# Kernel tuning notes

Hardware: AMD Instinct MI355X
Metric: run time of the kernel (lower is better)

Reference implementation:

```python
import jax, jax.numpy as jnp
import numpy as np
from jax import lax

S, B, W = 128, 64, 16          # sent_len, batch, word_len
V, CV = 50000, 100             # word vocab, char vocab
WE, CE, FN, CK = 300, 30, 4, 3 # word emb dim, char emb dim, char filter num, char kernel
C = 512                        # cnn_out_channel
NT = 20                        # number of tags
NL = 3                         # number of GLU conv layers
PAD = 0


def setup_inputs() -> dict:
    key = jax.random.key(0)
    ks = jax.random.split(key, 16)
    words = jax.random.randint(ks[0], (S, B), 1, V)          # no pads -> full CRF mask
    chars = jax.random.randint(ks[1], (B, S, W), 1, CV)
    tags = jax.random.randint(ks[2], (S, B), 0, NT)
    word_emb = jax.random.normal(ks[3], (V, WE), jnp.float32) * 0.1
    char_emb = jax.random.normal(ks[4], (CV, CE), jnp.float32) * 0.1
    char_cnn_w = jax.random.normal(ks[5], (CE * FN, 1, CK), jnp.float32) * 0.1  # grouped conv, groups=CE
    char_cnn_b = jax.random.normal(ks[6], (CE * FN,), jnp.float32) * 0.01
    lin_w = jax.random.normal(ks[7], (WE + CE * FN, C), jnp.float32) * 0.05
    lin_b = jax.random.normal(ks[8], (C,), jnp.float32) * 0.01
    conv_w = jax.random.normal(ks[9], (NL, 2 * C, C, 3), jnp.float32) * 0.03
    conv_b = jax.random.normal(ks[10], (NL, 2 * C), jnp.float32) * 0.01
    fc_w = jax.random.normal(ks[11], (C, NT), jnp.float32) * 0.05
    fc_b = jax.random.normal(ks[12], (NT,), jnp.float32) * 0.01
    crf_start = jax.random.normal(ks[13], (NT,), jnp.float32) * 0.1
    crf_end = jax.random.normal(ks[14], (NT,), jnp.float32) * 0.1
    crf_trans = jax.random.normal(ks[15], (NT, NT), jnp.float32) * 0.1
    return dict(words=words, chars=chars, tags=tags, word_emb=word_emb, char_emb=char_emb,
                char_cnn_w=char_cnn_w, char_cnn_b=char_cnn_b, lin_w=lin_w, lin_b=lin_b,
                conv_w=conv_w, conv_b=conv_b, fc_w=fc_w, fc_b=fc_b,
                crf_start=crf_start, crf_end=crf_end, crf_trans=crf_trans)


def _emissions(words, chars, word_emb, char_emb, char_cnn_w, char_cnn_b,
               lin_w, lin_b, conv_w, conv_b, fc_w, fc_b):
    s, b = words.shape
    # word embeddings: [S,B,WE]
    emb_out = word_emb[words]
    # char embeddings + batched grouped char-CNN (replaces the python loop over sent positions)
    ch = char_emb[chars]                                   # [B,S,W,CE]
    ch = ch.reshape(b * s, W, CE).transpose(0, 2, 1)       # [B*S, CE, W]
    co = lax.conv_general_dilated(ch, char_cnn_w, (1,), 'VALID',
                                  dimension_numbers=('NCH', 'OIH', 'NCH'),
                                  feature_group_count=CE)
    co = co + char_cnn_b[None, :, None]                    # [B*S, CE*FN, W-CK+1]
    cf = co.max(axis=2).reshape(b, s, CE * FN).transpose(1, 0, 2)  # [S,B,120]
    word_features = jnp.concatenate([emb_out, cf], axis=2)  # [S,B,420]
    # gated-CNN (GLU) encoder
    h = word_features @ lin_w + lin_b                      # [S,B,C]
    h = jnp.transpose(h, (1, 2, 0))                        # [B,C,S]
    scale = jnp.sqrt(jnp.asarray(0.5, h.dtype))
    for l in range(conv_w.shape[0]):
        c = lax.conv_general_dilated(h, conv_w[l], (1,), ((1, 1),),
                                     dimension_numbers=('NCH', 'OIH', 'NCH'))
        c = c + conv_b[l][None, :, None]                   # [B,2C,S]
        a, g = jnp.split(c, 2, axis=1)
        h = (a * jax.nn.sigmoid(g) + h) * scale            # GLU + residual + scale
    enc = jnp.transpose(h, (2, 0, 1))                      # [S,B,C]
    emis = enc @ fc_w + fc_b                               # [S,B,NT]
    mask = (words != PAD)                                  # [S,B]
    return emis, mask


def _crf_nll(emis, tags, mask, crf_start, crf_end, crf_trans):
    s, b, nt = emis.shape
    maskf = mask.astype(emis.dtype)
    bi = jnp.arange(b)
    # numerator: score of the gold path
    emis_sc = jnp.take_along_axis(emis, tags[:, :, None], axis=2)[..., 0]  # [S,B]
    trans_sc = crf_trans[tags[:-1], tags[1:]]                              # [S-1,B]
    num = crf_start[tags[0]] + emis_sc[0] + ((trans_sc + emis_sc[1:]) * maskf[1:]).sum(0)
    last_idx = mask.sum(0).astype(jnp.int32) - 1
    num = num + crf_end[tags[last_idx, bi]]
    # denominator: forward algorithm (sequential DP over time)
    alpha0 = crf_start[None, :] + emis[0]                  # [B,NT]
    def step(alpha, xs):
        e_t, m_t = xs
        nxt = jax.nn.logsumexp(alpha[:, :, None] + crf_trans[None] + e_t[:, None, :], axis=1)
        return jnp.where(m_t[:, None], nxt, alpha), None
    alpha, _ = lax.scan(step, alpha0, (emis[1:], mask[1:]))
    logz = jax.nn.logsumexp(alpha + crf_end[None, :], axis=1)
    return -(num - logz).sum()


def _viterbi(emis, mask, crf_start, crf_end, crf_trans):
    s, b, nt = emis.shape
    bi = jnp.arange(b)
    ident = jnp.broadcast_to(jnp.arange(nt)[None, :], (b, nt))
    score0 = crf_start[None, :] + emis[0]                  # [B,NT]
    def step(score, xs):
        e_t, m_t = xs
        brd = score[:, :, None] + crf_trans[None]          # [B,NT_prev,NT_cur]
        bp = jnp.argmax(brd, axis=1)                       # [B,NT]
        nxt = jnp.max(brd, axis=1) + e_t
        score = jnp.where(m_t[:, None], nxt, score)
        bp = jnp.where(m_t[:, None], bp, ident)
        return score, bp
    final, bps = lax.scan(step, score0, (emis[1:], mask[1:]))  # bps [S-1,B,NT]
    last_tag = jnp.argmax(final + crf_end[None, :], axis=1)    # [B]
    def back(tag, bp):
        prev = bp[bi, tag]
        return prev, tag
    first_tag, rest = lax.scan(back, last_tag, bps, reverse=True)  # rest: tags at 1..S-1
    return jnp.concatenate([first_tag[None], rest], axis=0).astype(jnp.int32)  # [S,B]


def reference(words, chars, tags, word_emb, char_emb, char_cnn_w, char_cnn_b,
              lin_w, lin_b, conv_w, conv_b, fc_w, fc_b, crf_start, crf_end, crf_trans):
    emis, mask = _emissions(words, chars, word_emb, char_emb, char_cnn_w, char_cnn_b,
                            lin_w, lin_b, conv_w, conv_b, fc_w, fc_b)
    crf_out = _viterbi(emis, mask, crf_start, crf_end, crf_trans)
    crf_loss = _crf_nll(emis, tags, mask, crf_start, crf_end, crf_trans)
    return crf_out, crf_loss
```

## Files before the change

### kernel.cpp

```cpp
#include <hip/hip_runtime.h>
#include <math.h>

typedef unsigned short ushort_t;
typedef short bf16x8 __attribute__((ext_vector_type(8)));
typedef float f32x4 __attribute__((ext_vector_type(4)));
typedef unsigned short u16x8 __attribute__((ext_vector_type(8)));

#define S_ 128
#define B_ 64
#define W_ 16
#define CE_ 30
#define FN_ 4
#define WE_ 300
#define FEAT_ 420
#define C_ 512
#define NT_ 20
#define KL_ 448

#define LOG2E_ 1.44269504088896340736f
#define LN2_   0.69314718055994530942f

#define EM_OFF   0
#define NLL_OFF  163840
#define H0_OFF   163968
#define HBUF_F   2129920
#define H1_OFF   (H0_OFF + HBUF_F)
#define WS_OFF   (H1_OFF + HBUF_F)
#define WSP_F    2359296
#define LW_OFF   (WS_OFF + WSP_F)
#define FS_OFF   (LW_OFF + 114688)
#define FW_OFF   (FS_OFF + 1835008)
#define WLAYER   (1024*1536)

__device__ __forceinline__ float b2f(ushort_t h) {
    unsigned u = ((unsigned)h) << 16;
    float f; __builtin_memcpy(&f, &u, 4); return f;
}
__device__ __forceinline__ ushort_t f2b(float f) {
    unsigned u; __builtin_memcpy(&u, &f, 4);
    unsigned r = (u + 0x7FFFu + ((u >> 16) & 1u)) >> 16;
    return (ushort_t)r;
}
__device__ __forceinline__ void gload16(const void* g, void* l) {
    __builtin_amdgcn_global_load_lds((const __attribute__((address_space(1))) void*)g,
                                     (__attribute__((address_space(3))) void*)l,
                                     16, 0, 0);
}

__global__ void k_embed(const int* __restrict__ words,
                        const float* __restrict__ word_emb,
                        const int* __restrict__ chars,
                        const float* __restrict__ char_emb,
                        const float* __restrict__ cw,
                        const float* __restrict__ cb,
                        ushort_t* __restrict__ Fh) {
    const int n = blockIdx.x;
    const int t = threadIdx.x;
    {
        int s = n >> 6, b = n & 63;
        int np = b * 128 + s;
        int wid = words[n];
        if (t < WE_ / 4) {
            float4 v = ((const float4*)(word_emb + (size_t)wid * WE_))[t];
            ushort4 o;
            o.x = f2b(v.x); o.y = f2b(v.y); o.z = f2b(v.z); o.w = f2b(v.w);
            *(ushort4*)(Fh + (size_t)np * KL_ + t * 4) = o;
        }
    }
    {
        int b = n >> 7, s = n & 127;
        int np = b * 128 + s;
        __shared__ int cidx[W_];
        if (t < W_) cidx[t] = chars[n * W_ + t];
        __syncthreads();
        if (t < CE_ * FN_) {
            int g = t >> 2;
            float w0 = cw[t*3+0], w1 = cw[t*3+1], w2 = cw[t*3+2];
            float x[W_];
            #pragma unroll
            for (int j = 0; j < W_; ++j) x[j] = char_emb[cidx[j] * CE_ + g];
            float m = -INFINITY;
            #pragma unroll
            for (int j = 0; j < W_ - 2; ++j) {
                float v = x[j]*w0 + x[j+1]*w1 + x[j+2]*w2;
                m = fmaxf(m, v);
            }
            Fh[(size_t)np * KL_ + WE_ + t] = f2b(m + cb[t]);
        }
        if (t < KL_ - FEAT_) Fh[(size_t)np * KL_ + FEAT_ + t] = 0;
    }
}

__global__ void k_prep(const float* __restrict__ conv_w, ushort_t* __restrict__ Wt,
                       const float* __restrict__ lin_w,  ushort_t* __restrict__ Lh,
                       const float* __restrict__ fc_w,   float* __restrict__ fwT,
                       ushort_t* __restrict__ h0, ushort_t* __restrict__ h1) {
    const int bid = blockIdx.x;
    const int t = threadIdx.x;
    if (bid < 18432) {
        size_t i = (size_t)bid * 256 + t;
        int ci = (int)(i & 511);
        int kr = (int)((i >> 9) % 3);
        size_t lo_ = i / 1536;
        Wt[i] = f2b(conv_w[lo_ * 1536 + (size_t)ci * 3 + kr]);
    } else if (bid < 19328) {
        int idx = (bid - 18432) * 256 + t;
        int c = idx / KL_, k = idx - c * KL_;
        float v = (k < FEAT_) ? lin_w[(size_t)k * C_ + c] : 0.f;
        Lh[idx] = f2b(v);
    } else if (bid < 19368) {
        int idx = (bid - 19328) * 256 + t;
        if (idx < NT_ * C_) {
            int j = idx >> 9, c = idx & 511;
            fwT[idx] = fc_w[(size_t)c * NT_ + j];
        }
    } else {
        int r = bid - 19368;
        int b = r >> 2, which = r & 3;
        ushort_t* buf = (which & 1) ? h1 : h0;
        int row = (which >> 1) ? 129 : 0;
        ((unsigned*)(buf + ((size_t)b * 130 + row) * 512))[t] = 0u;
    }
}

__global__ __launch_bounds__(256) void k_lin_gemm(
    const ushort_t* __restrict__ Lh, const ushort_t* __restrict__ Fh,
    const float* __restrict__ lb, ushort_t* __restrict__ Oh)
{
    __shared__ short lds[8192];
    short* AhS = lds;
    short* BhS = lds + 4096;

    const int bid = blockIdx.x;
    const int c0 = (bid & 3) << 7;
    const int n0 = (bid >> 2) << 7;
    const int t = threadIdx.x;
    const int w = t >> 6;
    const int lane = t & 63;
    const int wr = w >> 1, wc = w & 1;

    const int srow0 = (w << 5) + (lane >> 2);
    const int srow1 = srow0 + 16;
    const int j0 = (lane & 3) ^ ((srow0 >> 1) & 3);
    const int j1 = (lane & 3) ^ ((srow1 >> 1) & 3);
    const size_t aoff0 = (size_t)(c0 + srow0) * KL_ + j0 * 8;
    const size_t aoff1 = (size_t)(c0 + srow1) * KL_ + j1 * 8;
    const size_t boff0 = (size_t)(n0 + srow0) * KL_ + j0 * 8;
    const size_t boff1 = (size_t)(n0 + srow1) * KL_ + j1 * 8;
    const int wofs = w << 10;

    const int lr = lane & 15, kg = lane >> 4;
    int aro[4], bro[4];
    #pragma unroll
    for (int m = 0; m < 4; ++m) { int r = (wr << 6) + (m << 4) + lr; aro[m] = (r << 5) + ((kg ^ ((r >> 1) & 3)) << 3); }
    #pragma unroll
    for (int n = 0; n < 4; ++n) { int r = (wc << 6) + (n << 4) + lr; bro[n] = (r << 5) + ((kg ^ ((r >> 1) & 3)) << 3); }

    f32x4 acc[4][4];
    #pragma unroll
    for (int m = 0; m < 4; ++m)
        #pragma unroll
        for (int n = 0; n < 4; ++n) acc[m][n] = (f32x4){0.f, 0.f, 0.f, 0.f};

    for (int k0 = 0; k0 < KL_; k0 += 32) {
        gload16(Lh + aoff0 + k0, AhS + wofs);
        gload16(Lh + aoff1 + k0, AhS + wofs + 512);
        gload16(Fh + boff0 + k0, BhS + wofs);
        gload16(Fh + boff1 + k0, BhS + wofs + 512);
        __syncthreads();
        bf16x8 avh[4], bvh[4];
        #pragma unroll
        for (int m = 0; m < 4; ++m) avh[m] = *(const bf16x8*)(AhS + aro[m]);
        #pragma unroll
        for (int n = 0; n < 4; ++n) bvh[n] = *(const bf16x8*)(BhS + bro[n]);
        #pragma unroll
        for (int m = 0; m < 4; ++m)
            #pragma unroll
            for (int n = 0; n < 4; ++n)
                acc[m][n] = __builtin_amdgcn_mfma_f32_16x16x32_bf16(avh[m], bvh[n], acc[m][n], 0, 0, 0);
        __syncthreads();
    }

    #pragma unroll
    for (int m = 0; m < 4; ++m) {
        const int c = c0 + (wr << 6) + (m << 4) + (kg << 2);
        float4 bb = *(const float4*)(lb + c);
        #pragma unroll
        for (int n = 0; n < 4; ++n) {
            const int np = n0 + (wc << 6) + (n << 4) + lr;
            const int b = np >> 7, s = np & 127;
            ushort4 h4;
            h4.x = f2b(acc[m][n][0] + bb.x);
            h4.y = f2b(acc[m][n][1] + bb.y);
            h4.z = f2b(acc[m][n][2] + bb.z);
            h4.w = f2b(acc[m][n][3] + bb.w);
            *(ushort4*)(Oh + ((size_t)b * 130 + s + 1) * 512 + c) = h4;
        }
    }
}

#define CBUFS 16896
__global__ __launch_bounds__(256) void k_conv_gemm(
    const ushort_t* __restrict__ Wt, const ushort_t* __restrict__ Ht,
    const float* __restrict__ cb,
    ushort_t* __restrict__ Ot)
{
    __shared__ short lds2[2 * CBUFS];
    float* g_lds = (float*)lds2;

    const int bid  = blockIdx.x;
    const int co0  = (bid >> 6) << 6;
    const int b    = bid & 63;
    const int t    = threadIdx.x;
    const int w    = t >> 6;
    const int lane = t & 63;
    const int wr   = w >> 1;
    const int wc   = w & 1;

    const int srow0 = (w << 5) + (lane >> 2);
    const int srow1 = srow0 + 16;
    const int j0 = (lane & 3) ^ ((srow0 >> 1) & 3);
    const int j1 = (lane & 3) ^ ((srow1 >> 1) & 3);
    const int coA0 = (srow0 < 64) ? (co0 + srow0) : (512 + co0 + srow0 - 64);
    const int coA1 = (srow1 < 64) ? (co0 + srow1) : (512 + co0 + srow1 - 64);
    const size_t aoff0 = (size_t)coA0 * 1536 + j0 * 8;
    const size_t aoff1 = (size_t)coA1 * 1536 + j1 * 8;
    const int lrow = lane >> 2;
    const int wofs = w << 10;

    const int lr = lane & 15, kg = lane >> 4;
    int aro[4];
    #pragma unroll
    for (int m = 0; m < 4; ++m) { int r = (wr << 6) + (m << 4) + lr; aro[m] = (r << 5) + ((kg ^ ((r >> 1) & 3)) << 3); }
    int bro[3][4];
    #pragma unroll
    for (int kr = 0; kr < 3; ++kr)
        #pragma unroll
        for (int n = 0; n < 4; ++n) {
            int r = (wc << 6) + (n << 4) + lr + kr;
            bro[kr][n] = (r << 5) + ((kg ^ ((r >> 1) & 3)) << 3);
        }

    f32x4 acc[4][4];
    #pragma unroll
    for (int m = 0; m < 4; ++m)
        #pragma unroll
        for (int n = 0; n < 4; ++n) acc[m][n] = (f32x4){0.f, 0.f, 0.f, 0.f};

    {
        short* AS = lds2;
        short* BS = lds2 + 12288;
        #pragma unroll
        for (int kr = 0; kr < 3; ++kr) {
            gload16(Wt + aoff0 + kr * 512, AS + kr * 4096 + wofs);
            gload16(Wt + aoff1 + kr * 512, AS + kr * 4096 + wofs + 512);
        }
        for (int i = w; i < 9; i += 4) {
            const int rr = (i << 4) + lrow;
            const int sj = (lane & 3) ^ ((rr >> 1) & 3);
            gload16(Ht + ((size_t)b * 130 + rr) * 512 + sj * 8, BS + (i << 9));
        }
    }
    __syncthreads();

    for (int it = 0; it < 16; ++it) {
        const int cur = it & 1;
        if (it + 1 < 16) {
            const int ci0 = (it + 1) << 5;
            short* ASn = lds2 + (cur ^ 1) * CBUFS;
            short* BSn = ASn + 12288;
            #pragma unroll
            for (int kr = 0; kr < 3; ++kr) {
                gload16(Wt + aoff0 + kr * 512 + ci0, ASn + kr * 4096 + wofs);
                gload16(Wt + aoff1 + kr * 512 + ci0, ASn + kr * 4096 + wofs + 512);
            }
            for (int i = w; i < 9; i += 4) {
                const int rr = (i << 4) + lrow;
                const int sj = (lane & 3) ^ ((rr >> 1) & 3);
                gload16(Ht + ((size_t)b * 130 + rr) * 512 + ci0 + sj * 8, BSn + (i << 9));
            }
        }
        const short* AS = lds2 + cur * CBUFS;
        const short* BS = AS + 12288;
        #pragma unroll
        for (int kr = 0; kr < 3; ++kr) {
            const short* A_h = AS + kr * 4096;
            bf16x8 avh[4], bvh[4];
            #pragma unroll
            for (int m = 0; m < 4; ++m) avh[m] = *(const bf16x8*)(A_h + aro[m]);
            #pragma unroll
            for (int n = 0; n < 4; ++n) bvh[n] = *(const bf16x8*)(BS + bro[kr][n]);
            #pragma unroll
            for (int m = 0; m < 4; ++m)
                #pragma unroll
                for (int n = 0; n < 4; ++n)
                    acc[m][n] = __builtin_amdgcn_mfma_f32_16x16x32_bf16(avh[m], bvh[n], acc[m][n], 0, 0, 0);
        }
        __syncthreads();
    }

    const float rs = 0.70710678118654752f;
    if (wr == 1) {
        #pragma unroll
        for (int m = 0; m < 4; ++m) {
            const int co_l = (m << 4) + (kg << 2);
            float4 bg = *(const float4*)(cb + 512 + co0 + co_l);
            #pragma unroll
            for (int n = 0; n < 4; ++n) {
                const int s_l = (wc << 6) + (n << 4) + lr;
                float4 gv;
                gv.x = acc[m][n][0] + bg.x;
                gv.y = acc[m][n][1] + bg.y;
                gv.z = acc[m][n][2] + bg.z;
                gv.w = acc[m][n][3] + bg.w;
                *(float4*)&g_lds[s_l * 68 + co_l] = gv;
            }
        }
    }
    __syncthreads();
    if (wr == 0) {
        #pragma unroll
        for (int m = 0; m < 4; ++m) {
            const int co_l = (m << 4) + (kg << 2);
            float4 ba = *(const float4*)(cb + co0 + co_l);
            #pragma unroll
            for (int n = 0; n < 4; ++n) {
                const int s_l = (wc << 6) + (n << 4) + lr;
                float4 gv = *(const float4*)&g_lds[s_l * 68 + co_l];
                size_t dst = ((size_t)b * 130 + s_l + 1) * 512 + co0 + co_l;
                ushort4 rh = *(const ushort4*)(Ht + dst);
                float a0 = acc[m][n][0] + ba.x, g0 = gv.x;
                float a1 = acc[m][n][1] + ba.y, g1 = gv.y;
                float a2 = acc[m][n][2] + ba.z, g2 = gv.z;
                float a3 = acc[m][n][3] + ba.w, g3 = gv.w;
                ushort4 h4;
                h4.x = f2b((a0 / (1.f + expf(-g0)) + b2f(rh.x)) * rs);
                h4.y = f2b((a1 / (1.f + expf(-g1)) + b2f(rh.y)) * rs);
                h4.z = f2b((a2 / (1.f + expf(-g2)) + b2f(rh.z)) * rs);
                h4.w = f2b((a3 / (1.f + expf(-g3)) + b2f(rh.w)) * rs);
                *(ushort4*)(Ot + dst) = h4;
            }
        }
    }
}

__global__ __launch_bounds__(256) void k_emis3(const ushort_t* __restrict__ hh,
                                               const float* __restrict__ fwT,
                                               const float* __restrict__ fc_b,
                                               float* __restrict__ emis) {
    __shared__ short hlds[16 * 520];
    __shared__ float wlds[20 * 516];
    const int b  = blockIdx.y;
    const int sc = blockIdx.x;
    const int t  = threadIdx.x;
    const int w  = t >> 6, lane = t & 63;

    #pragma unroll
    for (int i = 0; i < 4; ++i) {
        int r = w * 4 + i;
        gload16(hh + ((size_t)b * 130 + sc * 16 + r + 1) * 512 + lane * 8,
                hlds + r * 520);
    }
    for (int idx = t; idx < 20 * 128; idx += 256) {
        int j = idx >> 7, cq = (idx & 127) << 2;
        *(float4*)&wlds[j * 516 + cq] = *(const float4*)(fwT + j * 512 + cq);
    }
    __syncthreads();

    #pragma unroll
    for (int pass = 0; pass < 2; ++pass) {
        int slot = t + pass * 256;
        if (slot < 16 * NT_) {
            int r = slot / NT_, j = slot - r * NT_;
            const short* hp = hlds + r * 520;
            const float* wp = wlds + j * 516;
            float acc = 0.f;
            for (int c0 = 0; c0 < 512; c0 += 8) {
                u16x8 hv = *(const u16x8*)(hp + c0);
                float4 w0 = *(const float4*)(wp + c0);
                float4 w1 = *(const float4*)(wp + c0 + 4);
                acc += b2f(hv[0])*w0.x + b2f(hv[1])*w0.y + b2f(hv[2])*w0.z + b2f(hv[3])*w0.w
                     + b2f(hv[4])*w1.x + b2f(hv[5])*w1.y + b2f(hv[6])*w1.z + b2f(hv[7])*w1.w;
            }
            int s = sc * 16 + r;
            emis[((size_t)s * B_ + b) * NT_ + j] = acc + fc_b[j];
        }
    }
}

#define VMAX(a, b) __builtin_elementwise_max((a), (b))
#define MAX20T(mx, a0, a1, a2, a3, a4) \
    { f32x4 mv_ = VMAX(VMAX(VMAX(a0, a1), VMAX(a2, a3)), a4); \
      mx = fmaxf(fmaxf(mv_[0], mv_[1]), fmaxf(mv_[2], mv_[3])); }
#define SEL(ov, oi, av, ai, bv2, bi2) \
    { bool g_ = (bv2) > (av); ov = g_ ? (bv2) : (av); oi = g_ ? (bi2) : (ai); }
#define ARGMAX20(best, bi, v0, v1, v2, v3, v4) \
    { float p0v,p1v,p2v,p3v,p4v,p5v,p6v,p7v,p8v,p9v; \
      int   p0i,p1i,p2i,p3i,p4i,p5i,p6i,p7i,p8i,p9i; \
      SEL(p0v,p0i, v0[0],0,  v0[1],1);  SEL(p1v,p1i, v0[2],2,  v0[3],3); \
      SEL(p2v,p2i, v1[0],4,  v1[1],5);  SEL(p3v,p3i, v1[2],6,  v1[3],7); \
      SEL(p4v,p4i, v2[0],8,  v2[1],9);  SEL(p5v,p5i, v2[2],10, v2[3],11); \
      SEL(p6v,p6i, v3[0],12, v3[1],13); SEL(p7v,p7i, v3[2],14, v3[3],15); \
      SEL(p8v,p8i, v4[0],16, v4[1],17); SEL(p9v,p9i, v4[2],18, v4[3],19); \
      float q0v,q1v,q2v,q3v,q4v; int q0i,q1i,q2i,q3i,q4i; \
      SEL(q0v,q0i,p0v,p0i,p1v,p1i); SEL(q1v,q1i,p2v,p2i,p3v,p3i); \
      SEL(q2v,q2i,p4v,p4i,p5v,p5i); SEL(q3v,q3i,p6v,p6i,p7v,p7i); \
      SEL(q4v,q4i,p8v,p8i,p9v,p9i); \
      float r0v,r1v; int r0i,r1i; \
      SEL(r0v,r0i,q0v,q0i,q1v,q1i); SEL(r1v,r1i,q2v,q2i,q3v,q3i); \
      float s0v; int s0i; \
      SEL(s0v,s0i,r0v,r0i,r1v,r1i); \
      SEL(best,bi,s0v,s0i,q4v,q4i); }
#define EXPC(d, s) d[0]=__builtin_amdgcn_exp2f(s[0]*LOG2E_); d[1]=__builtin_amdgcn_exp2f(s[1]*LOG2E_); \
                   d[2]=__builtin_amdgcn_exp2f(s[2]*LOG2E_); d[3]=__builtin_amdgcn_exp2f(s[3]*LOG2E_)
#define LGKM0() asm volatile("s_waitcnt lgkmcnt(0)" ::: "memory")

__global__ __launch_bounds__(256) void k_crf(const float* __restrict__ emis,
                                             const int* __restrict__ words,
                                             const int* __restrict__ tags,
                                             const float* __restrict__ tstart,
                                             const float* __restrict__ tend,
                                             const float* __restrict__ ttrans,
                                             float* __restrict__ nll,
                                             float* __restrict__ out) {
    __shared__ float e_lds[S_ * NT_];
    __shared__ float pe_lds[S_ * NT_];
    __shared__ int   P_lds[S_ * NT_];
    __shared__ float brA[32], brB[32], brC[32], brD[32];
    __shared__ float Fv[NT_], Gv[NT_], a63[NT_], g63[NT_];
    __shared__ float CfL, CbL;
    __shared__ int tag63L;
    const int b = blockIdx.x;
    const int t = threadIdx.x;
    const int w = t >> 6;
    const int ln = t & 63;

    for (int idx = t; idx < S_ * NT_; idx += 256) {
        int tt = idx / NT_, j = idx - tt * NT_;
        float ev = emis[((size_t)tt * B_ + b) * NT_ + j];
        e_lds[idx] = ev;
        pe_lds[idx] = __builtin_amdgcn_exp2f(ev * LOG2E_);
    }
    __syncthreads();

    unsigned long long mlo = __ballot(words[ln * B_ + b] != 0);
    unsigned long long mhi = __ballot(words[(64 + ln) * B_ + b] != 0);
    const bool act = ln < NT_;
    const int jc = act ? ln : 0;
    float part = 0.f;

    #define MBIT(tt) ((((tt) < 64 ? (mlo >> (tt)) : (mhi >> ((tt) - 64))) & 1ull) != 0)

    if (w == 0) {
        for (int tt = ln; tt < S_; tt += 64) {
            int tgc = tags[tt * B_ + b];
            bool m = MBIT(tt);
            if (tt == 0) {
                part += tstart[tgc] + e_lds[tgc];
            } else if (m) {
                int tgp = tags[(tt - 1) * B_ + b];
                part += ttrans[tgp * NT_ + tgc] + e_lds[tt * NT_ + tgc];
            }
        }
        #pragma unroll
        for (int o = 32; o >= 1; o >>= 1) part += __shfl_down(part, o);

        f32x4 t0, t1, t2, t3, t4;
        #define LDTC(v, q) v = (f32x4){ ttrans[(4*(q)+0)*NT_ + jc], ttrans[(4*(q)+1)*NT_ + jc], \
                                        ttrans[(4*(q)+2)*NT_ + jc], ttrans[(4*(q)+3)*NT_ + jc] }
        LDTC(t0, 0); LDTC(t1, 1); LDTC(t2, 2); LDTC(t3, 3); LDTC(t4, 4);
        f32x4 E0, E1, E2, E3, E4;
        EXPC(E0, t0); EXPC(E1, t1); EXPC(E2, t2); EXPC(E3, t3); EXPC(E4, t4);

        float a0own = tstart[jc] + e_lds[jc];
        if (act) brA[ln] = a0own;
        LGKM0();
        f32x4 a0 = *(const f32x4*)&brA[0];
        f32x4 a1 = *(const f32x4*)&brA[4];
        f32x4 a2 = *(const f32x4*)&brA[8];
        f32x4 a3 = *(const f32x4*)&brA[12];
        f32x4 a4 = *(const f32x4*)&brA[16];
        float m0; MAX20T(m0, a0, a1, a2, a3, a4);
        float beta = __builtin_amdgcn_exp2f((a0own - m0) * LOG2E_);
        int L2 = 0;
        for (int tt = 1; tt < 64; ++tt) {
            if (MBIT(tt)) {
                float pe = pe_lds[tt * NT_ + jc];
                if (act) brA[ln] = beta;
                LGKM0();
                f32x4 b0 = *(const f32x4*)&brA[0];
                f32x4 b1 = *(const f32x4*)&brA[4];
                f32x4 b2 = *(const f32x4*)&brA[8];
                f32x4 b3 = *(const f32x4*)&brA[12];
                f32x4 b4 = *(const f32x4*)&brA[16];
                float mx; MAX20T(mx, b0, b1, b2, b3, b4);
                f32x4 pr = b0 * E0 + b1 * E1 + b2 * E2 + b3 * E3 + b4 * E4;
                float dot = (pr[0] + pr[1]) + (pr[2] + pr[3]);
                unsigned bits; __builtin_memcpy(&bits, &mx, 4);
                int ex = (int)((bits >> 23) & 255u) - 127;
                unsigned rb = (unsigned)(127 - ex) << 23;
                float r; __builtin_memcpy(&r, &rb, 4);
                L2 += ex;
                beta = dot * r * pe;
            }
        }
        if (act) Fv[ln] = beta;
        if (ln == 0) CfL = m0 + (float)L2 * LN2_;
    } else if (w == 1) {
        f32x4 r0, r1, r2, r3, r4;
        #define LDTR(v, q) v = (f32x4){ ttrans[jc*NT_ + 4*(q)+0], ttrans[jc*NT_ + 4*(q)+1], \
                                        ttrans[jc*NT_ + 4*(q)+2], ttrans[jc*NT_ + 4*(q)+3] }
        LDTR(r0, 0); LDTR(r1, 1); LDTR(r2, 2); LDTR(r3, 3); LDTR(r4, 4);
        f32x4 E0, E1, E2, E3, E4;
        EXPC(E0, r0); EXPC(E1, r1); EXPC(E2, r2); EXPC(E3, r3); EXPC(E4, r4);
        f32x4 d0 = (f32x4){ tend[0],  tend[1],  tend[2],  tend[3]  };
        f32x4 d1 = (f32x4){ tend[4],  tend[5],  tend[6],  tend[7]  };
        f32x4 d2 = (f32x4){ tend[8],  tend[9],  tend[10], tend[11] };
        f32x4 d3 = (f32x4){ tend[12], tend[13], tend[14], tend[15] };
        f32x4 d4 = (f32x4){ tend[16], tend[17], tend[18], tend[19] };
        float mend; MAX20T(mend, d0, d1, d2, d3, d4);
        float G = __builtin_amdgcn_exp2f((tend[jc] - mend) * LOG2E_);
        int L2b = 0;
        for (int tt = 126; tt >= 63; --tt) {
            if (MBIT(tt + 1)) {
                float w_own = G * pe_lds[(tt + 1) * NT_ + jc];
                if (act) brB[ln] = w_own;
                LGKM0();
                f32x4 q0 = *(const f32x4*)&brB[0];
                f32x4 q1 = *(const f32x4*)&brB[4];
                f32x4 q2 = *(const f32x4*)&brB[8];
                f32x4 q3 = *(const f32x4*)&brB[12];
                f32x4 q4 = *(const f32x4*)&brB[16];
                float mx; MAX20T(mx, q0, q1, q2, q3, q4);
                f32x4 pr = q0 * E0 + q1 * E1 + q2 * E2 + q3 * E3 + q4 * E4;
                float dot = (pr[0] + pr[1]) + (pr[2] + pr[3]);
                unsigned bits; __builtin_memcpy(&bits, &mx, 4);
                int ex = (int)((bits >> 23) & 255u) - 127;
                unsigned rb = (unsigned)(127 - ex) << 23;
                float r; __builtin_memcpy(&r, &rb, 4);
                L2b += ex;
                G = dot * r;
            }
        }
        if (act) Gv[ln] = G;
        if (ln == 0) CbL = mend + (float)L2b * LN2_;
    } else if (w == 2) {
        f32x4 t0, t1, t2, t3, t4;
        LDTC(t0, 0); LDTC(t1, 1); LDTC(t2, 2); LDTC(t3, 3); LDTC(t4, 4);
        float sown = tstart[jc] + e_lds[jc];
        if (act) brC[ln] = sown;
        LGKM0();
        for (int tt = 1; tt < 64; ++tt) {
            float e = e_lds[tt * NT_ + jc];
            f32x4 a0 = *(const f32x4*)&brC[0];
            f32x4 a1 = *(const f32x4*)&brC[4];
            f32x4 a2 = *(const f32x4*)&brC[8];
            f32x4 a3 = *(const f32x4*)&brC[12];
            f32x4 a4 = *(const f32x4*)&brC[16];
            f32x4 v0 = a0 + t0, v1 = a1 + t1, v2 = a2 + t2, v3 = a3 + t3, v4 = a4 + t4;
            float best; int bi;
            ARGMAX20(best, bi, v0, v1, v2, v3, v4);
            bool m = MBIT(tt);
            float nxt = best + e;
            sown = m ? nxt : sown;
            if (act) {
                brC[ln] = sown;
                P_lds[tt * NT_ + ln] = m ? bi : ln;
            }
            LGKM0();
        }
        if (act) a63[ln] = sown;
    } else {
        f32x4 r0, r1, r2, r3, r4;
        LDTR(r0, 0); LDTR(r1, 1); LDTR(r2, 2); LDTR(r3, 3); LDTR(r4, 4);
        float gown = tend[jc];
        if (act) brD[ln] = gown + e_lds[127 * NT_ + jc];
        LGKM0();
        for (int tt = 126; tt >= 63; --tt) {
            f32x4 q0 = *(const f32x4*)&brD[0];
            f32x4 q1 = *(const f32x4*)&brD[4];
            f32x4 q2 = *(const f32x4*)&brD[8];
            f32x4 q3 = *(const f32x4*)&brD[12];
            f32x4 q4 = *(const f32x4*)&brD[16];
            f32x4 v0 = r0 + q0, v1 = r1 + q1, v2 = r2 + q2, v3 = r3 + q3, v4 = r4 + q4;
            float best; int bi;
            ARGMAX20(best, bi, v0, v1, v2, v3, v4);
            bool m = MBIT(tt + 1);
            gown = m ? best : gown;
            if (act) {
                P_lds[(tt + 1) * NT_ + ln] = m ? bi : ln;
                brD[ln] = gown + e_lds[tt * NT_ + jc];
            }
            LGKM0();
        }
        if (act) g63[ln] = gown;
    }
    __syncthreads();

    if (t == 0) {
        float zf = 0.f;
        #pragma unroll
        for (int j = 0; j < NT_; ++j) zf += Fv[j] * Gv[j];
        float logz = CfL + CbL + __builtin_amdgcn_logf(zf) * LN2_;
        int cnt = __popcll(mlo) + __popcll(mhi);
        float num = part + tend[tags[(cnt - 1) * B_ + b]];
        nll[b] = logz - num;
        float bv = a63[0] + g63[0]; int bt = 0;
        #pragma unroll
        for (int j = 1; j < NT_; ++j) {
            float v = a63[j] + g63[j];
            if (v > bv) { bv = v; bt = j; }
        }
        tag63L = bt;
    }
    __syncthreads();

    if (t == 128) {
        int tag = tag63L;
        out[63 * B_ + b] = (float)tag;
        for (int tt = 63; tt >= 1; --tt) {
            tag = P_lds[tt * NT_ + tag];
            out[(tt - 1) * B_ + b] = (float)tag;
        }
    }
    if (t == 192) {
        int tag = tag63L;
        for (int tt = 64; tt < 128; ++tt) {
            tag = P_lds[tt * NT_ + tag];
            out[tt * B_ + b] = (float)tag;
        }
    }
}

__global__ void k_loss(const float* __restrict__ nll, float* __restrict__ out) {
    float v = nll[threadIdx.x];
    #pragma unroll
    for (int o = 32; o >= 1; o >>= 1) v += __shfl_down(v, o);
    if (threadIdx.x == 0) out[S_ * B_] = v;
}

extern "C" void kernel_launch(void* const* d_in, const int* in_sizes, int n_in,
                              void* d_out, int out_size, void* d_ws, size_t ws_size,
                              hipStream_t stream) {
    (void)in_sizes; (void)n_in; (void)out_size; (void)ws_size;
    const int*   words     = (const int*)d_in[0];
    const int*   chars     = (const int*)d_in[1];
    const int*   tags      = (const int*)d_in[2];
    const float* word_emb  = (const float*)d_in[3];
    const float* char_emb  = (const float*)d_in[4];
    const float* ccw       = (const float*)d_in[5];
    const float* ccb       = (const float*)d_in[6];
    const float* lin_w     = (const float*)d_in[7];
    const float* lin_b     = (const float*)d_in[8];
    const float* conv_w    = (const float*)d_in[9];
    const float* conv_b    = (const float*)d_in[10];
    const float* fc_w      = (const float*)d_in[11];
    const float* fc_b      = (const float*)d_in[12];
    const float* crf_start = (const float*)d_in[13];
    const float* crf_end   = (const float*)d_in[14];
    const float* crf_trans = (const float*)d_in[15];

    float* ws   = (float*)d_ws;
    float* em   = ws + EM_OFF;
    float* nll  = ws + NLL_OFF;
    ushort_t* h0  = (ushort_t*)(ws + H0_OFF);
    ushort_t* h1  = (ushort_t*)(ws + H1_OFF);
    ushort_t* wsp = (ushort_t*)(ws + WS_OFF);
    ushort_t* lwp = (ushort_t*)(ws + LW_OFF);
    ushort_t* fsp = (ushort_t*)(ws + FS_OFF);
    float* fwT  = ws + FW_OFF;
    float* out  = (float*)d_out;

    k_embed<<<S_ * B_, 128, 0, stream>>>(words, word_emb, chars, char_emb, ccw, ccb, fsp);
    k_prep<<<19624, 256, 0, stream>>>(conv_w, wsp, lin_w, lwp, fc_w, fwT, h0, h1);
    k_lin_gemm<<<256, 256, 0, stream>>>(lwp, fsp, lin_b, h0);

    k_conv_gemm<<<512, 256, 0, stream>>>(wsp,              h0, conv_b,        h1);
    k_conv_gemm<<<512, 256, 0, stream>>>(wsp + WLAYER,     h1, conv_b + 1024, h0);
    k_conv_gemm<<<512, 256, 0, stream>>>(wsp + 2*WLAYER,   h0, conv_b + 2048, h1);

    k_emis3<<<dim3(8, B_), 256, 0, stream>>>(h1, fwT, fc_b, em);
    k_crf<<<B_, 256, 0, stream>>>(em, words, tags, crf_start, crf_end, crf_trans, nll, out);
    k_loss<<<1, 64, 0, stream>>>(nll, out);
}
```

Baseline: 173.9 us.

## Load conv GEMM weight fragments directly into registers instead of LDS

The GLU conv GEMM kernel stops staging the weight (A) tiles through shared memory. Each lane now reads its MFMA A fragments straight from global memory into a double-buffered register array, and only the activation (B) tiles stay double-buffered in LDS, which shrinks the shared-memory footprint. The aim is to cut LDS traffic and footprint, which could allow higher occupancy. The cost is more VGPRs (96 extra bf16x8 registers), a fully unrolled loop, and non-coalesced 16-byte global reads per lane that may expose load latency.

Result: slower. 252.7 us (+45.4%).

```diff
diff --git a/kernel.cpp b/kernel.cpp
--- a/kernel.cpp
+++ b/kernel.cpp
@@ -199,14 +199,13 @@
     }
 }
 
-#define CBUFS 16896
 __global__ __launch_bounds__(256) void k_conv_gemm(
     const ushort_t* __restrict__ Wt, const ushort_t* __restrict__ Ht,
     const float* __restrict__ cb,
     ushort_t* __restrict__ Ot)
 {
-    __shared__ short lds2[2 * CBUFS];
-    float* g_lds = (float*)lds2;
+    __shared__ short ldsB[17408];
+    float* g_lds = (float*)ldsB;
 
     const int bid  = blockIdx.x;
     const int co0  = (bid >> 6) << 6;
@@ -217,21 +216,16 @@
     const int wr   = w >> 1;
     const int wc   = w & 1;
 
-    const int srow0 = (w << 5) + (lane >> 2);
-    const int srow1 = srow0 + 16;
-    const int j0 = (lane & 3) ^ ((srow0 >> 1) & 3);
-    const int j1 = (lane & 3) ^ ((srow1 >> 1) & 3);
-    const int coA0 = (srow0 < 64) ? (co0 + srow0) : (512 + co0 + srow0 - 64);
-    const int coA1 = (srow1 < 64) ? (co0 + srow1) : (512 + co0 + srow1 - 64);
-    const size_t aoff0 = (size_t)coA0 * 1536 + j0 * 8;
-    const size_t aoff1 = (size_t)coA1 * 1536 + j1 * 8;
     const int lrow = lane >> 2;
-    const int wofs = w << 10;
-
     const int lr = lane & 15, kg = lane >> 4;
-    int aro[4];
-    #pragma unroll
-    for (int m = 0; m < 4; ++m) { int r = (wr << 6) + (m << 4) + lr; aro[m] = (r << 5) + ((kg ^ ((r >> 1) & 3)) << 3); }
+
+    const ushort_t* aP[4];
+    #pragma unroll
+    for (int m = 0; m < 4; ++m) {
+        int r = (wr << 6) + (m << 4) + lr;
+        int coA = (r < 64) ? (co0 + r) : (512 + co0 + r - 64);
+        aP[m] = Wt + (size_t)coA * 1536 + kg * 8;
+    }
     int bro[3][4];
     #pragma unroll
     for (int kr = 0; kr < 3; ++kr)
@@ -247,54 +241,48 @@
         #pragma unroll
         for (int n = 0; n < 4; ++n) acc[m][n] = (f32x4){0.f, 0.f, 0.f, 0.f};
 
-    {
-        short* AS = lds2;
-        short* BS = lds2 + 12288;
-        #pragma unroll
-        for (int kr = 0; kr < 3; ++kr) {
-            gload16(Wt + aoff0 + kr * 512, AS + kr * 4096 + wofs);
-            gload16(Wt + aoff1 + kr * 512, AS + kr * 4096 + wofs + 512);
-        }
-        for (int i = w; i < 9; i += 4) {
-            const int rr = (i << 4) + lrow;
-            const int sj = (lane & 3) ^ ((rr >> 1) & 3);
-            gload16(Ht + ((size_t)b * 130 + rr) * 512 + sj * 8, BS + (i << 9));
-        }
+    bf16x8 av[2][3][4];
+    #pragma unroll
+    for (int kr = 0; kr < 3; ++kr)
+        #pragma unroll
+        for (int m = 0; m < 4; ++m)
+            av[0][kr][m] = *(const bf16x8*)(aP[m] + kr * 512);
+
+    for (int i = w; i < 9; i += 4) {
+        const int rr = (i << 4) + lrow;
+        const int sj = (lane & 3) ^ ((rr >> 1) & 3);
+        gload16(Ht + ((size_t)b * 130 + rr) * 512 + sj * 8, ldsB + (i << 9));
     }
     __syncthreads();
 
+    #pragma unroll
     for (int it = 0; it < 16; ++it) {
         const int cur = it & 1;
         if (it + 1 < 16) {
-            const int ci0 = (it + 1) << 5;
-            short* ASn = lds2 + (cur ^ 1) * CBUFS;
-            short* BSn = ASn + 12288;
-            #pragma unroll
-            for (int kr = 0; kr < 3; ++kr) {
-                gload16(Wt + aoff0 + kr * 512 + ci0, ASn + kr * 4096 + wofs);
-                gload16(Wt + aoff1 + kr * 512 + ci0, ASn + kr * 4096 + wofs + 512);
-            }
+            const int ci0n = (it + 1) << 5;
+            short* BSn = ldsB + (cur ^ 1) * 4608;
             for (int i = w; i < 9; i += 4) {
                 const int rr = (i << 4) + lrow;
                 const int sj = (lane & 3) ^ ((rr >> 1) & 3);
-                gload16(Ht + ((size_t)b * 130 + rr) * 512 + ci0 + sj * 8, BSn + (i << 9));
-            }
-        }
-        const short* AS = lds2 + cur * CBUFS;
-        const short* BS = AS + 12288;
+                gload16(Ht + ((size_t)b * 130 + rr) * 512 + ci0n + sj * 8, BSn + (i << 9));
+            }
+            #pragma unroll
+            for (int kr = 0; kr < 3; ++kr)
+                #pragma unroll
+                for (int m = 0; m < 4; ++m)
+                    av[cur ^ 1][kr][m] = *(const bf16x8*)(aP[m] + kr * 512 + ci0n);
+        }
+        const short* BS = ldsB + cur * 4608;
         #pragma unroll
         for (int kr = 0; kr < 3; ++kr) {
-            const short* A_h = AS + kr * 4096;
-            bf16x8 avh[4], bvh[4];
-            #pragma unroll
-            for (int m = 0; m < 4; ++m) avh[m] = *(const bf16x8*)(A_h + aro[m]);
+            bf16x8 bvh[4];
             #pragma unroll
             for (int n = 0; n < 4; ++n) bvh[n] = *(const bf16x8*)(BS + bro[kr][n]);
             #pragma unroll
             for (int m = 0; m < 4; ++m)
                 #pragma unroll
                 for (int n = 0; n < 4; ++n)
-                    acc[m][n] = __builtin_amdgcn_mfma_f32_16x16x32_bf16(avh[m], bvh[n], acc[m][n], 0, 0, 0);
+                    acc[m][n] = __builtin_amdgcn_mfma_f32_16x16x32_bf16(av[cur][kr][m], bvh[n], acc[m][n], 0, 0, 0);
         }
         __syncthreads();
     }
```
